# Kernel optimization log

Measured on AMD Instinct MI355X. Metric: run time of the kernel, lower is better.

Reference implementation:

```python
import jax, jax.numpy as jnp
import numpy as np
import math

B, S, D, H, F, E, K, L, V = 1, 2048, 768, 12, 1536, 8, 2, 2, 32000


def _ln(x, w, b, eps=1e-5):
    m = x.mean(-1, keepdims=True)
    v = ((x - m) ** 2).mean(-1, keepdims=True)
    return (x - m) / jnp.sqrt(v + eps) * w + b


def setup_inputs() -> dict:
    key = jax.random.key(0)
    ks = jax.random.split(key, 16)
    std = 0.02
    inp = {
        'tokens': jax.random.randint(ks[0], (B, S), 0, V),
        'emb': jax.random.normal(ks[1], (V, D), jnp.float32) * std,
        'qkv_w': jax.random.normal(ks[2], (L, 3 * D, D), jnp.float32) * std,
        'qkv_b': jax.random.normal(ks[3], (L, 3 * D), jnp.float32) * std,
        'out_w': jax.random.normal(ks[4], (L, D, D), jnp.float32) * std,
        'out_b': jax.random.normal(ks[5], (L, D), jnp.float32) * std,
        'ln1_w': jnp.ones((L, D), jnp.float32),
        'ln1_b': jax.random.normal(ks[6], (L, D), jnp.float32) * std,
        'ln2_w': jnp.ones((L, D), jnp.float32),
        'ln2_b': jax.random.normal(ks[7], (L, D), jnp.float32) * std,
        'gate_w': jax.random.normal(ks[8], (L, E, D), jnp.float32) * std,
        'eg_w': jax.random.normal(ks[9], (L, E, F, D), jnp.float32) * std,
        'eu_w': jax.random.normal(ks[10], (L, E, F, D), jnp.float32) * std,
        'ed_w': jax.random.normal(ks[11], (L, E, D, F), jnp.float32) * std,
        'rms_w': jnp.ones((D,), jnp.float32),
    }
    return inp


def reference(tokens, emb, qkv_w, qkv_b, out_w, out_b, ln1_w, ln1_b,
              ln2_w, ln2_b, gate_w, eg_w, eu_w, ed_w, rms_w):
    Dh = D // H
    x = emb[tokens] * math.sqrt(D)  # (B,S,D)
    for l in range(L):
        # --- MultiheadAttention (batch_first, no mask, eval) ---
        qkv = x @ qkv_w[l].T + qkv_b[l]
        q, k, v = jnp.split(qkv, 3, axis=-1)
        q = q.reshape(B, S, H, Dh).transpose(0, 2, 1, 3)
        k = k.reshape(B, S, H, Dh).transpose(0, 2, 1, 3)
        v = v.reshape(B, S, H, Dh).transpose(0, 2, 1, 3)
        att = jax.nn.softmax(jnp.einsum('bhqd,bhkd->bhqk', q, k) / math.sqrt(Dh), axis=-1)
        o = jnp.einsum('bhqk,bhkd->bhqd', att, v).transpose(0, 2, 1, 3).reshape(B, S, D)
        o = o @ out_w[l].T + out_b[l]
        x = _ln(x + o, ln1_w[l], ln1_b[l])
        # --- SimpleDeepseekV3MoE: top-k gate, softmax over top-k scores ---
        gs = jnp.einsum('bsd,ed->bse', x, gate_w[l])
        topv, topi = jax.lax.top_k(gs, K)
        tw = jax.nn.softmax(topv, axis=-1)  # (B,S,K)
        # dense per-expert combine weight (0 for unselected experts)
        ew = jnp.sum(jax.nn.one_hot(topi, E, dtype=x.dtype) * tw[..., None], axis=-2)  # (B,S,E)
        hg = jax.nn.silu(jnp.einsum('bsd,efd->bsef', x, eg_w[l]))
        hu = jnp.einsum('bsd,efd->bsef', x, eu_w[l])
        ye = jnp.einsum('bsef,edf->bsed', hg * hu, ed_w[l])
        moe = jnp.einsum('bsed,bse->bsd', ye, ew)
        x = _ln(x + moe, ln2_w[l], ln2_b[l])
    # final RMSNorm (torch default eps=None -> finfo eps)
    rms = jnp.sqrt(jnp.mean(x * x, axis=-1, keepdims=True) + jnp.finfo(x.dtype).eps)
    x = x / rms * rms_w
    logits = x @ emb.T  # tied lm_head
    return logits
```

## Files before the change

### kernel.cpp

```cpp
#include <hip/hip_runtime.h>

#define SQ   2048
#define DM   768
#define NHD  12
#define DHD  64
#define FF   1536
#define NE   8
#define NL   2
#define NV   32000

typedef __attribute__((ext_vector_type(8))) short bf16x8;
typedef __attribute__((ext_vector_type(4))) float f32x4;

__device__ __forceinline__ unsigned short f2bf(float f) {
  unsigned u = __float_as_uint(f);
  return (unsigned short)((u + 0x7fffu + ((u >> 16) & 1u)) >> 16);
}
__device__ __forceinline__ float bf2f(unsigned short h) {
  return __uint_as_float(((unsigned)h) << 16);
}

#define GLD16(ldsp, gp) __builtin_amdgcn_global_load_lds( \
    (const __attribute__((address_space(1))) void*)(gp),  \
    (__attribute__((address_space(3))) void*)(ldsp), 16, 0, 0)

__device__ __forceinline__ void conv8(const float* s, unsigned short* d) {
  float4 a = *(const float4*)s;
  float4 b = *(const float4*)(s + 4);
  int4 pk = make_int4(
      (int)((unsigned)f2bf(a.x) | ((unsigned)f2bf(a.y) << 16)),
      (int)((unsigned)f2bf(a.z) | ((unsigned)f2bf(a.w) << 16)),
      (int)((unsigned)f2bf(b.x) | ((unsigned)f2bf(b.y) << 16)),
      (int)((unsigned)f2bf(b.z) | ((unsigned)f2bf(b.w) << 16)));
  *(int4*)d = pk;
}

__global__ __launch_bounds__(256) void conv_k(const float* __restrict__ s,
    unsigned short* __restrict__ d) {
  size_t i = (size_t)(blockIdx.x * 256 + threadIdx.x) * 8;
  conv8(s + i, d + i);
}

__global__ __launch_bounds__(256) void conv3_k(const float* __restrict__ s0,
    const float* __restrict__ s1, const float* __restrict__ s2,
    unsigned short* __restrict__ d, int per) {
  int b = blockIdx.x;
  const float* s = (b < per) ? s0 : (b < 2 * per) ? s1 : s2;
  int sb = (b < per) ? b : (b < 2 * per) ? b - per : b - 2 * per;
  size_t di = (size_t)b * 2048 + threadIdx.x * 8;
  size_t si = (size_t)sb * 2048 + threadIdx.x * 8;
  conv8(s + si, d + di);
}

__global__ __launch_bounds__(256) void conv2_k(const float* __restrict__ s0,
    const float* __restrict__ s1, unsigned short* __restrict__ d, int per0) {
  int b = blockIdx.x;
  const float* s = (b < per0) ? s0 : s1;
  int sb = (b < per0) ? b : b - per0;
  size_t di = (size_t)b * 2048 + threadIdx.x * 8;
  size_t si = (size_t)sb * 2048 + threadIdx.x * 8;
  conv8(s + si, d + di);
}

__global__ __launch_bounds__(256) void embed_k(const int* __restrict__ tok,
    const float* __restrict__ emb, float* __restrict__ x,
    unsigned short* __restrict__ xbf, int* __restrict__ cnt) {
  if (blockIdx.x == 0 && threadIdx.x < NE) cnt[threadIdx.x] = 0;
  int idx = blockIdx.x * 256 + threadIdx.x;
  int s = idx / DM, d = idx % DM;
  float v = emb[(size_t)tok[s] * DM + d] * 27.712812921102035f;
  x[idx] = v;
  xbf[idx] = f2bf(v);
}

__global__ __launch_bounds__(512, 1) void gemmr_k(
    const unsigned short* __restrict__ A, long long lda,
    const unsigned short* __restrict__ B, long long ldb,
    float* __restrict__ C, long long ldc,
    int Kd, int mT)
{
  int nwg = gridDim.x, bid = blockIdx.x;
  int q = nwg >> 3, r = nwg & 7;
  int xcd = bid & 7, j = bid >> 3;
  int wid = (xcd < r ? xcd * (q + 1) : r * (q + 1) + (xcd - r) * q) + j;
  int mt = wid % mT, nt = wid / mT;
  int m0 = mt * 256, n0 = nt * 256;

  __shared__ __align__(16) unsigned short lds[4][2][8192];

  int t = threadIdx.x, w = t >> 6, lane = t & 63;
  int wm = w >> 2, wn = w & 3;
  int fr = lane & 15, ksg = lane >> 4;

  int srow = t >> 2;
  int schunk = ((t & 3) ^ ((srow >> 1) & 3)) * 8;
  const unsigned short* sa0 = A + (size_t)(m0 +       srow) * lda + schunk;
  const unsigned short* sa1 = A + (size_t)(m0 + 128 + srow) * lda + schunk;
  const unsigned short* sb0 = B + (size_t)(n0 +       srow) * ldb + schunk;
  const unsigned short* sb1 = B + (size_t)(n0 + 128 + srow) * ldb + schunk;
  int wofs = w * 512;

  int NS = Kd >> 5;
  f32x4 acc[8][4] = {};

#define STAGEV(s) { \
    int sl_ = (s) & 3; \
    long long ko_ = (long long)((s) >> 1) * 64 + ((s) & 1) * 32; \
    GLD16(&lds[sl_][0][wofs], sa0 + ko_); \
    GLD16(&lds[sl_][0][4096 + wofs], sa1 + ko_); \
    GLD16(&lds[sl_][1][wofs], sb0 + ko_); \
    GLD16(&lds[sl_][1][4096 + wofs], sb1 + ko_); }

  STAGEV(0);
  STAGEV(1);
  asm volatile("s_waitcnt vmcnt(4)" ::: "memory");
  __builtin_amdgcn_s_barrier();
  __builtin_amdgcn_sched_barrier(0);

  int ko = (ksg ^ ((fr >> 1) & 3)) * 8;
  for (int s = 0; s < NS; ++s) {
    int slot = s & 3;
    const unsigned short* Al = &lds[slot][0][0];
    const unsigned short* Bl = &lds[slot][1][0];
    bf16x8 af[8], bf[4];
    #pragma unroll
    for (int m = 0; m < 8; ++m)
      af[m] = *(const bf16x8*)&Al[(wm * 128 + m * 16 + fr) * 32 + ko];
    #pragma unroll
    for (int n = 0; n < 4; ++n)
      bf[n] = *(const bf16x8*)&Bl[(wn * 64 + n * 16 + fr) * 32 + ko];
    if (s + 2 < NS) STAGEV(s + 2);
    asm volatile("s_waitcnt lgkmcnt(0)" ::: "memory");
    __builtin_amdgcn_sched_barrier(0);
    __builtin_amdgcn_s_setprio(1);
    #pragma unroll
    for (int m = 0; m < 8; ++m)
      #pragma unroll
      for (int n = 0; n < 4; ++n)
        acc[m][n] = __builtin_amdgcn_mfma_f32_16x16x32_bf16(
            af[m], bf[n], acc[m][n], 0, 0, 0);
    __builtin_amdgcn_s_setprio(0);
    if (s + 1 < NS) {
      if (s + 2 < NS) asm volatile("s_waitcnt vmcnt(4)" ::: "memory");
      else            asm volatile("s_waitcnt vmcnt(0)" ::: "memory");
      __builtin_amdgcn_s_barrier();
      __builtin_amdgcn_sched_barrier(0);
    }
  }
#undef STAGEV

  int rb = ksg * 4;
  #pragma unroll
  for (int M = 0; M < 8; ++M)
    #pragma unroll
    for (int n = 0; n < 4; ++n)
      #pragma unroll
      for (int rr = 0; rr < 4; ++rr)
        C[(size_t)(m0 + wm * 128 + M * 16 + rb + rr) * ldc +
          (n0 + wn * 64 + n * 16 + fr)] = acc[M][n][rr];
}

template<bool GATHER, bool OBF16>
__global__ __launch_bounds__(512) void gemm256_k(
    const unsigned short* __restrict__ A, long long lda,
    const unsigned short* __restrict__ B, long long ldb, long long b_z,
    void* __restrict__ C, long long ldc, long long c_z,
    int M, int Kd, int mT, int nT, int Z, int zmod,
    const int* __restrict__ glist, long long gl_z,
    const int* __restrict__ cnt)
{
  int nwg = gridDim.x, bid = blockIdx.x;
  int q = nwg >> 3, r = nwg & 7;
  int xcd = bid & 7, j = bid >> 3;
  int wid = (xcd < r ? xcd * (q + 1) : r * (q + 1) + (xcd - r) * q) + j;
  int z = wid % Z; int rem = wid / Z;
  int mt = rem % mT, nt = rem / mT;
  int zz = z % zmod;
  int Mz = cnt ? cnt[zz] : M;
  int m0 = mt * 128, n0 = nt * 256;
  if (m0 >= Mz) return;
  (void)nT;

  const unsigned short* Bz = B + (size_t)z * b_z;

  __shared__ __align__(16) unsigned short lds[3 * 6 * 4096];

  int t = threadIdx.x, w = t >> 6, lane = t & 63;
  int wm = (w >> 2) * 64, wn = (w & 3) * 64;
  int fr = lane & 15, ksg = lane >> 4;
  int lrow = lane >> 3;
  int lchunk = ((lane & 7) ^ lrow) * 8;

  const unsigned short* sp[6];
  #pragma unroll
  for (int hh = 0; hh < 2; ++hh) {
    int gr = m0 + hh * 64 + w * 8 + lrow; if (gr >= Mz) gr = Mz - 1;
    int arow;
    if constexpr (GATHER) arow = glist[(size_t)zz * gl_z + gr]; else arow = gr;
    sp[hh] = A + (size_t)arow * lda + lchunk;
  }
  #pragma unroll
  for (int hh = 0; hh < 4; ++hh)
    sp[2 + hh] = Bz + (size_t)(n0 + hh * 64 + w * 8 + lrow) * ldb + lchunk;

  int rdA = (w >> 2) * 4096;
  int rdB = (2 + (w & 3)) * 4096;
  int stDst = w * 512;

  int rx = fr & 7;
  int off0 = (ksg ^ rx) * 8;
  int off1 = ((4 + ksg) ^ rx) * 8;

  int KT = Kd >> 6;
  f32x4 acc[4][4] = {};

  #pragma unroll
  for (int h = 0; h < 6; ++h)
    GLD16(&lds[h * 4096 + stDst], sp[h]);
  #pragma unroll
  for (int h = 0; h < 6; ++h)
    GLD16(&lds[(6 + h) * 4096 + stDst], sp[h] + 64);
  asm volatile("s_waitcnt vmcnt(6)" ::: "memory");
  __builtin_amdgcn_s_barrier();
  __builtin_amdgcn_sched_barrier(0);

  int buf = 0;
  for (int kt = 0; kt < KT; ++kt) {
    const unsigned short* Abl = &lds[buf * 6 * 4096 + rdA];
    const unsigned short* Bbl = &lds[buf * 6 * 4096 + rdB];
    int pf = (kt + 2 < KT);
    int pbuf = buf + 2; if (pbuf >= 3) pbuf -= 3;
    unsigned short* pd = &lds[pbuf * 6 * 4096 + stDst];
    long long koff = (long long)(kt + 2) * 64;

    if (pf) {
      GLD16(pd + 0 * 4096, sp[0] + koff);
      GLD16(pd + 1 * 4096, sp[1] + koff);
      GLD16(pd + 2 * 4096, sp[2] + koff);
    }
    {
      bf16x8 af[4], bv[4];
      #pragma unroll
      for (int m = 0; m < 4; ++m)
        af[m] = *(const bf16x8*)&Abl[(m * 16 + fr) * 64 + off0];
      #pragma unroll
      for (int n = 0; n < 4; ++n)
        bv[n] = *(const bf16x8*)&Bbl[(n * 16 + fr) * 64 + off0];
      __builtin_amdgcn_s_setprio(1);
      #pragma unroll
      for (int m = 0; m < 4; ++m)
        #pragma unroll
        for (int n = 0; n < 4; ++n)
          acc[m][n] = __builtin_amdgcn_mfma_f32_16x16x32_bf16(
              af[m], bv[n], acc[m][n], 0, 0, 0);
      __builtin_amdgcn_s_setprio(0);
    }
    if (pf) {
      GLD16(pd + 3 * 4096, sp[3] + koff);
      GLD16(pd + 4 * 4096, sp[4] + koff);
      GLD16(pd + 5 * 4096, sp[5] + koff);
    }
    {
      bf16x8 af[4], bv[4];
      #pragma unroll
      for (int m = 0; m < 4; ++m)
        af[m] = *(const bf16x8*)&Abl[(m * 16 + fr) * 64 + off1];
      #pragma unroll
      for (int n = 0; n < 4; ++n)
        bv[n] = *(const bf16x8*)&Bbl[(n * 16 + fr) * 64 + off1];
      __builtin_amdgcn_s_setprio(1);
      #pragma unroll
      for (int m = 0; m < 4; ++m)
        #pragma unroll
        for (int n = 0; n < 4; ++n)
          acc[m][n] = __builtin_amdgcn_mfma_f32_16x16x32_bf16(
              af[m], bv[n], acc[m][n], 0, 0, 0);
      __builtin_amdgcn_s_setprio(0);
    }
    if (pf) {
      asm volatile("s_waitcnt vmcnt(6)" ::: "memory");
    } else if (kt + 1 < KT) {
      asm volatile("s_waitcnt vmcnt(0)" ::: "memory");
    }
    __builtin_amdgcn_s_barrier();
    __builtin_amdgcn_sched_barrier(0);
    buf = buf + 1; if (buf == 3) buf = 0;
  }

  int rb = ksg * 4;
  #pragma unroll
  for (int m = 0; m < 4; ++m) {
    #pragma unroll
    for (int n = 0; n < 4; ++n) {
      #pragma unroll
      for (int rr = 0; rr < 4; ++rr) {
        int row = m0 + wm + m * 16 + rb + rr;
        if (row >= Mz) continue;
        size_t off = (size_t)z * c_z + (size_t)row * ldc +
                     (n0 + wn + n * 16 + fr);
        if constexpr (OBF16) ((unsigned short*)C)[off] = f2bf(acc[m][n][rr]);
        else                 ((float*)C)[off] = acc[m][n][rr];
      }
    }
  }
}

template<bool GATHER, bool BIAS, bool OBF16, bool VT>
__global__ __launch_bounds__(256) void gemm_k(
    const unsigned short* __restrict__ A, long long lda, long long a_z,
    const unsigned short* __restrict__ B, long long ldb, long long b_z,
    const float* __restrict__ bias,
    void* __restrict__ C, long long ldc, long long c_z,
    int M, int N, int Kd, float scale,
    const int* __restrict__ glist, long long gl_z,
    const int* __restrict__ cnt, int mT, int nT, int Z,
    unsigned short* __restrict__ vtout)
{
  int nwg = gridDim.x, bid = blockIdx.x;
  int q = nwg >> 3, r = nwg & 7;
  int xcd = bid & 7, j = bid >> 3;
  int wid = (xcd < r ? xcd * (q + 1) : r * (q + 1) + (xcd - r) * q) + j;
  int z = wid % Z; int rem = wid / Z;
  int mt = rem % mT, nt = rem / mT;

  int Mz = cnt ? cnt[z] : M;
  int m0 = mt * 128, n0 = nt * 128;
  if (m0 >= Mz) return;

  const unsigned short* Ab = A + (size_t)z * a_z;
  const unsigned short* Bb = B + (size_t)z * b_z;

  __shared__ __align__(16) unsigned short As[128 * 64];
  __shared__ __align__(16) unsigned short Bs[128 * 64];

  int t = threadIdx.x, w = t >> 6, lane = t & 63;
  int wm = (w >> 1) * 64, wn = (w & 1) * 64;
  int fr = lane & 15, ksg = lane >> 4;
  int lrow = lane >> 3;
  int lchunk = ((lane & 7) ^ lrow) * 8;

  const unsigned short* ap[4];
  const unsigned short* bp[4];
  unsigned short* la[4];
  unsigned short* lb[4];
  #pragma unroll
  for (int i = 0; i < 4; ++i) {
    int rrow = w * 32 + i * 8 + lrow;
    int gr = m0 + rrow; if (gr >= Mz) gr = Mz - 1;
    int arow; if constexpr (GATHER) arow = glist[(size_t)z * gl_z + gr]; else arow = gr;
    ap[i] = Ab + (size_t)arow * lda + lchunk;
    int br = n0 + rrow; if (br >= N) br = N - 1;
    bp[i] = Bb + (size_t)br * ldb + lchunk;
    la[i] = &As[(w * 32 + i * 8) * 64];
    lb[i] = &Bs[(w * 32 + i * 8) * 64];
  }

  int rx = fr & 7;
  int off0 = ((0 + ksg) ^ rx) * 8;
  int off1 = ((4 + ksg) ^ rx) * 8;

  f32x4 acc[4][4] = {};

  for (int k0 = 0; k0 < Kd; k0 += 64) {
    #pragma unroll
    for (int i = 0; i < 4; ++i) GLD16(la[i], ap[i] + k0);
    #pragma unroll
    for (int i = 0; i < 4; ++i) GLD16(lb[i], bp[i] + k0);
    __syncthreads();
    #pragma unroll
    for (int kb = 0; kb < 2; ++kb) {
      int offk = kb ? off1 : off0;
      bf16x8 af[4], bv[4];
      #pragma unroll
      for (int m = 0; m < 4; ++m)
        af[m] = *(const bf16x8*)&As[(wm + m * 16 + fr) * 64 + offk];
      #pragma unroll
      for (int n = 0; n < 4; ++n)
        bv[n] = *(const bf16x8*)&Bs[(wn + n * 16 + fr) * 64 + offk];
      #pragma unroll
      for (int m = 0; m < 4; ++m)
        #pragma unroll
        for (int n = 0; n < 4; ++n)
          acc[m][n] = __builtin_amdgcn_mfma_f32_16x16x32_bf16(
              af[m], bv[n], acc[m][n], 0, 0, 0);
    }
    __syncthreads();
  }

  int rb = ksg * 4;
  #pragma unroll
  for (int m = 0; m < 4; ++m) {
    #pragma unroll
    for (int n = 0; n < 4; ++n) {
      int col = n0 + wn + n * 16 + fr;
      if (col >= N) continue;
      #pragma unroll
      for (int rr = 0; rr < 4; ++rr) {
        int row = m0 + wm + m * 16 + rb + rr;
        if (row >= Mz) continue;
        float v = acc[m][n][rr] * scale;
        if constexpr (BIAS) v += bias[col];
        size_t off = (size_t)z * c_z + (size_t)row * ldc + col;
        if constexpr (OBF16) ((unsigned short*)C)[off] = f2bf(v);
        else                 ((float*)C)[off] = v;
        if constexpr (VT) {
          if (n0 >= 2 * DM)
            vtout[(size_t)(col - 2 * DM) * SQ + row] = f2bf(v);
        }
      }
    }
  }
}

__global__ __launch_bounds__(128) void flash_k(
    const unsigned short* __restrict__ qkv,
    const unsigned short* __restrict__ vt,
    unsigned short* __restrict__ o)
{
  int nwg = gridDim.x, bid = blockIdx.x;
  int cpx = nwg >> 3;
  int wid = (bid & 7) * cpx + (bid >> 3);
  int h  = wid >> 6;
  int qt = wid & 63;
  int q0 = qt * 32;

  __shared__ __align__(16) unsigned short Ks[128 * 64];
  __shared__ __align__(16) unsigned short Vs[128 * 64];
  __shared__ __align__(16) unsigned short Ps[2][16 * 136];

  int t = threadIdx.x, w = t >> 6, lane = t & 63;
  int fr = lane & 15, ksg = lane >> 4;
  int lrow = lane >> 3;
  int lchunk = ((lane & 7) ^ lrow) * 8;

  const unsigned short* qbase = qkv + (size_t)q0 * (3 * DM) + h * DHD;
  #pragma unroll
  for (int i = 0; i < 2; ++i) {
    int rrow = w * 16 + i * 8 + lrow;
    GLD16(&Ks[(w * 16 + i * 8) * 64], qbase + (size_t)rrow * (3 * DM) + lchunk);
  }
  __syncthreads();
  bf16x8 qf[2];
  {
    int row = w * 16 + fr, ph = fr & 7;
    qf[0] = *(const bf16x8*)&Ks[row * 64 + ((ksg ^ ph) * 8)];
    qf[1] = *(const bf16x8*)&Ks[row * 64 + (((4 + ksg) ^ ph) * 8)];
  }
  __syncthreads();

  const unsigned short* kbase = qkv + DM + h * DHD;
  const unsigned short* vb = vt + (size_t)(h * DHD) * SQ;

  f32x4 oacc[4] = {};
  float m_r[4] = {-1e30f, -1e30f, -1e30f, -1e30f};
  float l_r[4] = {0.f, 0.f, 0.f, 0.f};

  for (int kt = 0; kt < SQ / 128; ++kt) {
    int kk0 = kt * 128;
    #pragma unroll
    for (int i = 0; i < 8; ++i) {
      int rrow = w * 64 + i * 8 + lrow;
      GLD16(&Ks[(w * 64 + i * 8) * 64],
            kbase + (size_t)(kk0 + rrow) * (3 * DM) + lchunk);
    }
    #pragma unroll
    for (int i = 0; i < 8; ++i) {
      int p = w * 64 + i * 8 + lrow;
      GLD16(&Vs[(w * 64 + i * 8) * 64],
            vb + (size_t)(p >> 1) * SQ + kk0 + (p & 1) * 64 + lchunk);
    }
    __syncthreads();

    f32x4 sacc[8] = {};
    #pragma unroll
    for (int kb = 0; kb < 2; ++kb) {
      #pragma unroll
      for (int n = 0; n < 8; ++n) {
        int row = n * 16 + fr;
        bf16x8 bvv = *(const bf16x8*)&Ks[row * 64 +
            (((kb * 4 + ksg) ^ (fr & 7)) * 8)];
        sacc[n] = __builtin_amdgcn_mfma_f32_16x16x32_bf16(
            qf[kb], bvv, sacc[n], 0, 0, 0);
      }
    }

    #pragma unroll
    for (int r = 0; r < 4; ++r) {
      float mx = sacc[0][r];
      #pragma unroll
      for (int n = 1; n < 8; ++n) mx = fmaxf(mx, sacc[n][r]);
      mx = fmaxf(mx, __shfl_xor(mx, 1));
      mx = fmaxf(mx, __shfl_xor(mx, 2));
      mx = fmaxf(mx, __shfl_xor(mx, 4));
      mx = fmaxf(mx, __shfl_xor(mx, 8));
      float mn = fmaxf(m_r[r], mx * 0.125f);
      float resc = __expf(m_r[r] - mn);
      m_r[r] = mn;
      #pragma unroll
      for (int n = 0; n < 4; ++n) oacc[n][r] *= resc;
      float rs = 0.f;
      #pragma unroll
      for (int n = 0; n < 8; ++n) {
        float p = __expf(sacc[n][r] * 0.125f - mn);
        rs += p;
        Ps[w][(ksg * 4 + r) * 136 + n * 16 + fr] = f2bf(p);
      }
      rs += __shfl_xor(rs, 1);
      rs += __shfl_xor(rs, 2);
      rs += __shfl_xor(rs, 4);
      rs += __shfl_xor(rs, 8);
      l_r[r] = l_r[r] * resc + rs;
    }

    #pragma unroll
    for (int ksi = 0; ksi < 4; ++ksi) {
      bf16x8 pa = *(const bf16x8*)&Ps[w][fr * 136 + ksi * 32 + ksg * 8];
      #pragma unroll
      for (int n = 0; n < 4; ++n) {
        int p = (n * 16 + fr) * 2 + (ksi >> 1);
        int c = (ksi & 1) * 4 + ksg;
        bf16x8 bvv = *(const bf16x8*)&Vs[p * 64 + ((c ^ (p & 7)) * 8)];
        oacc[n] = __builtin_amdgcn_mfma_f32_16x16x32_bf16(
            pa, bvv, oacc[n], 0, 0, 0);
      }
    }
    __syncthreads();
  }

  unsigned short* ob = o + (size_t)(q0 + w * 16) * DM + h * DHD;
  #pragma unroll
  for (int r = 0; r < 4; ++r) {
    float invl = 1.f / l_r[r];
    int qrow = ksg * 4 + r;
    #pragma unroll
    for (int n = 0; n < 4; ++n)
      ob[(size_t)qrow * DM + n * 16 + fr] = f2bf(oacc[n][r] * invl);
  }
}

__global__ __launch_bounds__(256) void add_ln_gate_k(const float* __restrict__ xin,
    const float* __restrict__ add, const float* __restrict__ w,
    const float* __restrict__ b, const float* __restrict__ gw,
    float* __restrict__ xout, unsigned short* __restrict__ xbf,
    float* __restrict__ tw, int* __restrict__ ti, int* __restrict__ cnt,
    int* __restrict__ lists, int* __restrict__ slot) {
  int row = blockIdx.x, t = threadIdx.x;
  const float* xi = xin + (size_t)row * DM;
  const float* ai = add + (size_t)row * DM;
  float v[3]; float s = 0.f, sq = 0.f;
  #pragma unroll
  for (int i = 0; i < 3; ++i) {
    int idx = t + i * 256;
    v[i] = xi[idx] + ai[idx];
    s += v[i]; sq += v[i] * v[i];
  }
  #pragma unroll
  for (int o = 32; o; o >>= 1) { s += __shfl_xor(s, o); sq += __shfl_xor(sq, o); }
  __shared__ float rsm[4], rqm[4];
  __shared__ float gsm[4][NE];
  int wv = t >> 6, lane = t & 63;
  if (lane == 0) { rsm[wv] = s; rqm[wv] = sq; }
  __syncthreads();
  s = rsm[0] + rsm[1] + rsm[2] + rsm[3];
  sq = rqm[0] + rqm[1] + rqm[2] + rqm[3];
  float mean = s * (1.f / 768.f);
  float var = sq * (1.f / 768.f) - mean * mean;
  float inv = rsqrtf(var + 1e-5f);
  float* xo = xout + (size_t)row * DM;
  unsigned short* xb = xbf + (size_t)row * DM;
  float y[3];
  #pragma unroll
  for (int i = 0; i < 3; ++i) {
    int idx = t + i * 256;
    y[i] = (v[i] - mean) * inv * w[idx] + b[idx];
    xo[idx] = y[i]; xb[idx] = f2bf(y[i]);
  }
  float p[NE];
  #pragma unroll
  for (int e = 0; e < NE; ++e) {
    p[e] = y[0] * gw[e * DM + t] + y[1] * gw[e * DM + t + 256]
         + y[2] * gw[e * DM + t + 512];
    #pragma unroll
    for (int o = 32; o; o >>= 1) p[e] += __shfl_xor(p[e], o);
  }
  if (lane == 0) {
    #pragma unroll
    for (int e = 0; e < NE; ++e) gsm[wv][e] = p[e];
  }
  __syncthreads();
  if (t == 0) {
    float v0 = -1e30f, v1 = -1e30f; int i0 = 0, i1 = 0;
    #pragma unroll
    for (int e = 0; e < NE; ++e) {
      float g = gsm[0][e] + gsm[1][e] + gsm[2][e] + gsm[3][e];
      if (g > v0) { v1 = v0; i1 = i0; v0 = g; i0 = e; }
      else if (g > v1) { v1 = g; i1 = e; }
    }
    float e1 = expf(v1 - v0);
    float invs = 1.f / (1.f + e1);
    tw[row * 2] = invs; tw[row * 2 + 1] = e1 * invs;
    ti[row * 2] = i0;   ti[row * 2 + 1] = i1;
    int p0 = atomicAdd(&cnt[i0], 1); lists[i0 * SQ + p0] = row; slot[row * 2] = p0;
    int p1 = atomicAdd(&cnt[i1], 1); lists[i1 * SQ + p1] = row; slot[row * 2 + 1] = p1;
  }
}

__global__ __launch_bounds__(256) void silu_mul_k(unsigned short* __restrict__ hg,
    const unsigned short* __restrict__ hu, const int* __restrict__ cnt) {
  int e = blockIdx.y, sl = blockIdx.x;
  if (sl >= cnt[e]) return;
  size_t base = ((size_t)e * SQ + sl) * FF;
  int t = threadIdx.x;
  #pragma unroll
  for (int i = 0; i < FF / 256; ++i) {
    size_t idx = base + t + i * 256;
    float g = bf2f(hg[idx]);
    float u = bf2f(hu[idx]);
    float sv = g / (1.f + expf(-g));
    hg[idx] = f2bf(sv * u);
  }
}

__global__ __launch_bounds__(256) void combine_ln_k(const float* __restrict__ xin,
    const float* __restrict__ ye, const float* __restrict__ tw,
    const int* __restrict__ ti, const int* __restrict__ slot,
    const float* __restrict__ w, const float* __restrict__ b,
    float* __restrict__ xout, unsigned short* __restrict__ xbf,
    int* __restrict__ cnt) {
  int row = blockIdx.x, t = threadIdx.x;
  if (row < NE && t == 0) cnt[row] = 0;
  int e0 = ti[row * 2], e1 = ti[row * 2 + 1];
  int p0 = slot[row * 2], p1 = slot[row * 2 + 1];
  float w0 = tw[row * 2], w1 = tw[row * 2 + 1];
  const float* y0 = ye + ((size_t)e0 * SQ + p0) * DM;
  const float* y1 = ye + ((size_t)e1 * SQ + p1) * DM;
  const float* xi = xin + (size_t)row * DM;
  float v[3]; float s = 0.f, sq = 0.f;
  #pragma unroll
  for (int i = 0; i < 3; ++i) {
    int idx = t + i * 256;
    v[i] = xi[idx] + w0 * y0[idx] + w1 * y1[idx];
    s += v[i]; sq += v[i] * v[i];
  }
  #pragma unroll
  for (int o = 32; o; o >>= 1) { s += __shfl_xor(s, o); sq += __shfl_xor(sq, o); }
  __shared__ float rsm[4], rqm[4];
  int wv = t >> 6;
  if ((t & 63) == 0) { rsm[wv] = s; rqm[wv] = sq; }
  __syncthreads();
  s = rsm[0] + rsm[1] + rsm[2] + rsm[3];
  sq = rqm[0] + rqm[1] + rqm[2] + rqm[3];
  float mean = s * (1.f / 768.f);
  float var = sq * (1.f / 768.f) - mean * mean;
  float inv = rsqrtf(var + 1e-5f);
  float* xo = xout + (size_t)row * DM;
  unsigned short* xb = xbf + (size_t)row * DM;
  #pragma unroll
  for (int i = 0; i < 3; ++i) {
    int idx = t + i * 256;
    float y = (v[i] - mean) * inv * w[idx] + b[idx];
    xo[idx] = y; xb[idx] = f2bf(y);
  }
}

__global__ __launch_bounds__(256) void rms_k(const float* __restrict__ x,
    const float* __restrict__ rw, unsigned short* __restrict__ xbf) {
  int row = blockIdx.x, t = threadIdx.x;
  const float* xi = x + (size_t)row * DM;
  float v[3]; float sq = 0.f;
  #pragma unroll
  for (int i = 0; i < 3; ++i) {
    int idx = t + i * 256;
    v[i] = xi[idx];
    sq += v[i] * v[i];
  }
  #pragma unroll
  for (int o = 32; o; o >>= 1) sq += __shfl_xor(sq, o);
  __shared__ float rqm[4];
  int wv = t >> 6;
  if ((t & 63) == 0) rqm[wv] = sq;
  __syncthreads();
  sq = rqm[0] + rqm[1] + rqm[2] + rqm[3];
  float inv = rsqrtf(sq * (1.f / 768.f) + 1.1920929e-07f);
  unsigned short* xb = xbf + (size_t)row * DM;
  #pragma unroll
  for (int i = 0; i < 3; ++i) {
    int idx = t + i * 256;
    xb[idx] = f2bf(v[i] * inv * rw[idx]);
  }
}

extern "C" void kernel_launch(void* const* d_in, const int* in_sizes, int n_in,
                              void* d_out, int out_size, void* d_ws, size_t ws_size,
                              hipStream_t stream) {
  (void)in_sizes; (void)n_in; (void)out_size; (void)ws_size;
  const int*   tokens = (const int*)d_in[0];
  const float* emb    = (const float*)d_in[1];
  const float* qkv_w  = (const float*)d_in[2];
  const float* qkv_b  = (const float*)d_in[3];
  const float* out_w  = (const float*)d_in[4];
  const float* out_b  = (const float*)d_in[5];
  const float* ln1_w  = (const float*)d_in[6];
  const float* ln1_b  = (const float*)d_in[7];
  const float* ln2_w  = (const float*)d_in[8];
  const float* ln2_b  = (const float*)d_in[9];
  const float* gate_w = (const float*)d_in[10];
  const float* eg_w   = (const float*)d_in[11];
  const float* eu_w   = (const float*)d_in[12];
  const float* ed_w   = (const float*)d_in[13];
  const float* rms_w  = (const float*)d_in[14];
  float* out = (float*)d_out;

  char* wsb = (char*)d_ws;
  float*          x_f    = (float*)(wsb + 0);
  unsigned short* x_bf   = (unsigned short*)(wsb + 6291456);
  unsigned short* qkv_bf = (unsigned short*)(wsb + 9437184);
  unsigned short* vt     = (unsigned short*)(wsb + 18874368);
  unsigned short* o_bf   = (unsigned short*)(wsb + 22020096);
  float*          tmp_f  = (float*)(wsb + 25165824);
  float*          tw     = (float*)(wsb + 31457280);
  int*            ti     = (int*)(wsb + 31473664);
  int*            cnt    = (int*)(wsb + 31490048);
  int*            lists  = (int*)(wsb + 31490304);
  int*            slot   = (int*)(wsb + 31555840);
  unsigned short* emb_bf = (unsigned short*)(wsb + 31572224);
  unsigned short* wbf    = (unsigned short*)(wsb + 80724224);
  unsigned short* hg     = (unsigned short*)(wsb + 142065920);
  unsigned short* hu     = (unsigned short*)(wsb + 142065920 + 50331648);
  float*          ye     = (float*)(wsb + 142065920 + 50331648);

  unsigned short* qw_bf = wbf;
  unsigned short* ow_bf = wbf + 1769472;
  unsigned short* eg_bf = wbf + 2359296;
  unsigned short* ed_bf = wbf + 21233664;

  conv_k<<<12000, 256, 0, stream>>>(emb, emb_bf);
  embed_k<<<SQ * DM / 256, 256, 0, stream>>>(tokens, emb, x_f, x_bf, cnt);

  for (int l = 0; l < NL; ++l) {
    const float* qw = qkv_w + (size_t)l * 3 * DM * DM;
    const float* qb = qkv_b + (size_t)l * 3 * DM;
    const float* ob = out_b + (size_t)l * DM;
    const float* ow = out_w + (size_t)l * DM * DM;
    const float* gw = gate_w + (size_t)l * NE * DM;
    const float* egw = eg_w + (size_t)l * NE * FF * DM;
    const float* euw = eu_w + (size_t)l * NE * FF * DM;
    const float* edw = ed_w + (size_t)l * NE * DM * FF;

    conv2_k<<<1152, 256, 0, stream>>>(qw, ow, qw_bf, 864);
    conv3_k<<<13824, 256, 0, stream>>>(egw, euw, edw, eg_bf, 4608);

    gemm_k<false, true, true, true><<<16 * 18, 256, 0, stream>>>(
        x_bf, DM, 0, qw_bf, DM, 0, qb, qkv_bf, 3 * DM, 0,
        SQ, 3 * DM, DM, 1.f, nullptr, 0, nullptr, 16, 18, 1, vt);

    flash_k<<<NHD * 64, 128, 0, stream>>>(qkv_bf, vt, o_bf);

    gemm_k<false, true, false, false><<<16 * 6, 256, 0, stream>>>(
        o_bf, DM, 0, ow_bf, DM, 0, ob, tmp_f, DM, 0,
        SQ, DM, DM, 1.f, nullptr, 0, nullptr, 16, 6, 1, nullptr);

    add_ln_gate_k<<<SQ, 256, 0, stream>>>(x_f, tmp_f, ln1_w + l * DM,
        ln1_b + l * DM, gw, x_f, x_bf, tw, ti, cnt, lists, slot);

    gemm256_k<true, true><<<16 * 6 * 16, 512, 0, stream>>>(
        x_bf, DM, eg_bf, DM, (long long)FF * DM,
        hg, FF, (long long)SQ * FF,
        SQ, DM, 16, 6, 16, 8, lists, SQ, cnt);

    silu_mul_k<<<dim3(SQ, NE), 256, 0, stream>>>(hg, hu, cnt);

    gemm_k<false, false, false, false><<<16 * 6 * NE, 256, 0, stream>>>(
        hg, FF, (long long)SQ * FF, ed_bf, FF, (long long)DM * FF, nullptr,
        ye, DM, (long long)SQ * DM,
        SQ, DM, FF, 1.f, nullptr, 0, cnt, 16, 6, NE, nullptr);

    combine_ln_k<<<SQ, 256, 0, stream>>>(x_f, ye, tw, ti, slot,
                                         ln2_w + l * DM, ln2_b + l * DM,
                                         x_f, x_bf, cnt);
  }

  rms_k<<<SQ, 256, 0, stream>>>(x_f, rms_w, x_bf);

  gemmr_k<<<8 * 125, 512, 0, stream>>>(
      x_bf, DM, emb_bf, DM, out, NV, DM, 8);
}
```

Before: 783.0 us.

## Batch weight conversion, move QKV and down-proj to 256-wide GEMM, fuse RMSNorm

Weight fp32->bf16 conversion for both layers is hoisted into single upfront launches instead of per-layer launches. The QKV projection and expert down-projection now use the larger 256-column tile GEMM, which gains bias and V-transpose epilogue support. silu_mul is collapsed to one block per row that loops over experts. The final RMSNorm is fused into the last combine+LayerNorm kernel. The intent is fewer launches and better GEMM efficiency. The trade-offs are larger workspace use and fewer workgroups for the down-projection grid.

```diff
diff --git a/kernel.cpp b/kernel.cpp
--- a/kernel.cpp
+++ b/kernel.cpp
@@ -41,12 +41,15 @@
   conv8(s + i, d + i);
 }
 
-__global__ __launch_bounds__(256) void conv3_k(const float* __restrict__ s0,
+__global__ __launch_bounds__(256) void conv4_k(const float* __restrict__ s0,
     const float* __restrict__ s1, const float* __restrict__ s2,
-    unsigned short* __restrict__ d, int per) {
+    const float* __restrict__ s3, unsigned short* __restrict__ d, int per) {
   int b = blockIdx.x;
-  const float* s = (b < per) ? s0 : (b < 2 * per) ? s1 : s2;
-  int sb = (b < per) ? b : (b < 2 * per) ? b - per : b - 2 * per;
+  const float* s; int sb;
+  if (b < per)          { s = s0; sb = b; }
+  else if (b < 2 * per) { s = s1; sb = b - per; }
+  else if (b < 3 * per) { s = s2; sb = b - 2 * per; }
+  else                  { s = s3; sb = b - 3 * per; }
   size_t di = (size_t)b * 2048 + threadIdx.x * 8;
   size_t si = (size_t)sb * 2048 + threadIdx.x * 8;
   conv8(s + si, d + di);
@@ -160,11 +163,13 @@
           (n0 + wn * 64 + n * 16 + fr)] = acc[M][n][rr];
 }
 
-template<bool GATHER, bool OBF16>
+template<bool GATHER, bool OBF16, bool BIAS, bool VT>
 __global__ __launch_bounds__(512) void gemm256_k(
-    const unsigned short* __restrict__ A, long long lda,
+    const unsigned short* __restrict__ A, long long lda, long long a_z,
     const unsigned short* __restrict__ B, long long ldb, long long b_z,
+    const float* __restrict__ bias,
     void* __restrict__ C, long long ldc, long long c_z,
+    unsigned short* __restrict__ vtout,
     int M, int Kd, int mT, int nT, int Z, int zmod,
     const int* __restrict__ glist, long long gl_z,
     const int* __restrict__ cnt)
@@ -181,6 +186,7 @@
   if (m0 >= Mz) return;
   (void)nT;
 
+  const unsigned short* Az = A + (size_t)z * a_z;
   const unsigned short* Bz = B + (size_t)z * b_z;
 
   __shared__ __align__(16) unsigned short lds[3 * 6 * 4096];
@@ -197,7 +203,7 @@
     int gr = m0 + hh * 64 + w * 8 + lrow; if (gr >= Mz) gr = Mz - 1;
     int arow;
     if constexpr (GATHER) arow = glist[(size_t)zz * gl_z + gr]; else arow = gr;
-    sp[hh] = A + (size_t)arow * lda + lchunk;
+    sp[hh] = Az + (size_t)arow * lda + lchunk;
   }
   #pragma unroll
   for (int hh = 0; hh < 4; ++hh)
@@ -292,20 +298,26 @@
   for (int m = 0; m < 4; ++m) {
     #pragma unroll
     for (int n = 0; n < 4; ++n) {
+      int col = n0 + wn + n * 16 + fr;
       #pragma unroll
       for (int rr = 0; rr < 4; ++rr) {
         int row = m0 + wm + m * 16 + rb + rr;
         if (row >= Mz) continue;
-        size_t off = (size_t)z * c_z + (size_t)row * ldc +
-                     (n0 + wn + n * 16 + fr);
-        if constexpr (OBF16) ((unsigned short*)C)[off] = f2bf(acc[m][n][rr]);
-        else                 ((float*)C)[off] = acc[m][n][rr];
+        float v = acc[m][n][rr];
+        if constexpr (BIAS) v += bias[col];
+        size_t off = (size_t)z * c_z + (size_t)row * ldc + col;
+        if constexpr (OBF16) ((unsigned short*)C)[off] = f2bf(v);
+        else                 ((float*)C)[off] = v;
+        if constexpr (VT) {
+          if (n0 >= 2 * DM)
+            vtout[(size_t)(col - 2 * DM) * SQ + row] = f2bf(v);
+        }
       }
     }
   }
 }
 
-template<bool GATHER, bool BIAS, bool OBF16, bool VT>
+template<bool GATHER, bool BIAS, bool OBF16>
 __global__ __launch_bounds__(256) void gemm_k(
     const unsigned short* __restrict__ A, long long lda, long long a_z,
     const unsigned short* __restrict__ B, long long ldb, long long b_z,
@@ -313,8 +325,7 @@
     void* __restrict__ C, long long ldc, long long c_z,
     int M, int N, int Kd, float scale,
     const int* __restrict__ glist, long long gl_z,
-    const int* __restrict__ cnt, int mT, int nT, int Z,
-    unsigned short* __restrict__ vtout)
+    const int* __restrict__ cnt, int mT, int nT, int Z)
 {
   int nwg = gridDim.x, bid = blockIdx.x;
   int q = nwg >> 3, r = nwg & 7;
@@ -403,10 +414,6 @@
         size_t off = (size_t)z * c_z + (size_t)row * ldc + col;
         if constexpr (OBF16) ((unsigned short*)C)[off] = f2bf(v);
         else                 ((float*)C)[off] = v;
-        if constexpr (VT) {
-          if (n0 >= 2 * DM)
-            vtout[(size_t)(col - 2 * DM) * SQ + row] = f2bf(v);
-        }
       }
     }
   }
@@ -607,28 +614,32 @@
 
 __global__ __launch_bounds__(256) void silu_mul_k(unsigned short* __restrict__ hg,
     const unsigned short* __restrict__ hu, const int* __restrict__ cnt) {
-  int e = blockIdx.y, sl = blockIdx.x;
-  if (sl >= cnt[e]) return;
-  size_t base = ((size_t)e * SQ + sl) * FF;
-  int t = threadIdx.x;
-  #pragma unroll
-  for (int i = 0; i < FF / 256; ++i) {
-    size_t idx = base + t + i * 256;
-    float g = bf2f(hg[idx]);
-    float u = bf2f(hu[idx]);
-    float sv = g / (1.f + expf(-g));
-    hg[idx] = f2bf(sv * u);
-  }
-}
-
+  int sl = blockIdx.x, t = threadIdx.x;
+  for (int e = 0; e < NE; ++e) {
+    if (sl < cnt[e]) {
+      size_t base = ((size_t)e * SQ + sl) * FF;
+      #pragma unroll
+      for (int i = 0; i < FF / 256; ++i) {
+        size_t idx = base + t + i * 256;
+        float g = bf2f(hg[idx]);
+        float u = bf2f(hu[idx]);
+        float sv = g / (1.f + expf(-g));
+        hg[idx] = f2bf(sv * u);
+      }
+    }
+  }
+}
+
+template<bool FINAL>
 __global__ __launch_bounds__(256) void combine_ln_k(const float* __restrict__ xin,
     const float* __restrict__ ye, const float* __restrict__ tw,
     const int* __restrict__ ti, const int* __restrict__ slot,
     const float* __restrict__ w, const float* __restrict__ b,
+    const float* __restrict__ rw,
     float* __restrict__ xout, unsigned short* __restrict__ xbf,
     int* __restrict__ cnt) {
   int row = blockIdx.x, t = threadIdx.x;
-  if (row < NE && t == 0) cnt[row] = 0;
+  if (!FINAL && row < NE && t == 0) cnt[row] = 0;
   int e0 = ti[row * 2], e1 = ti[row * 2 + 1];
   int p0 = slot[row * 2], p1 = slot[row * 2 + 1];
   float w0 = tw[row * 2], w1 = tw[row * 2 + 1];
@@ -653,40 +664,34 @@
   float mean = s * (1.f / 768.f);
   float var = sq * (1.f / 768.f) - mean * mean;
   float inv = rsqrtf(var + 1e-5f);
-  float* xo = xout + (size_t)row * DM;
   unsigned short* xb = xbf + (size_t)row * DM;
+  float y[3];
   #pragma unroll
   for (int i = 0; i < 3; ++i) {
     int idx = t + i * 256;
-    float y = (v[i] - mean) * inv * w[idx] + b[idx];
-    xo[idx] = y; xb[idx] = f2bf(y);
-  }
-}
-
-__global__ __launch_bounds__(256) void rms_k(const float* __restrict__ x,
-    const float* __restrict__ rw, unsigned short* __restrict__ xbf) {
-  int row = blockIdx.x, t = threadIdx.x;
-  const float* xi = x + (size_t)row * DM;
-  float v[3]; float sq = 0.f;
-  #pragma unroll
-  for (int i = 0; i < 3; ++i) {
-    int idx = t + i * 256;
-    v[i] = xi[idx];
-    sq += v[i] * v[i];
-  }
-  #pragma unroll
-  for (int o = 32; o; o >>= 1) sq += __shfl_xor(sq, o);
-  __shared__ float rqm[4];
-  int wv = t >> 6;
-  if ((t & 63) == 0) rqm[wv] = sq;
-  __syncthreads();
-  sq = rqm[0] + rqm[1] + rqm[2] + rqm[3];
-  float inv = rsqrtf(sq * (1.f / 768.f) + 1.1920929e-07f);
-  unsigned short* xb = xbf + (size_t)row * DM;
-  #pragma unroll
-  for (int i = 0; i < 3; ++i) {
-    int idx = t + i * 256;
-    xb[idx] = f2bf(v[i] * inv * rw[idx]);
+    y[i] = (v[i] - mean) * inv * w[idx] + b[idx];
+  }
+  if constexpr (!FINAL) {
+    float* xo = xout + (size_t)row * DM;
+    #pragma unroll
+    for (int i = 0; i < 3; ++i) {
+      int idx = t + i * 256;
+      xo[idx] = y[i]; xb[idx] = f2bf(y[i]);
+    }
+  } else {
+    float sq2 = y[0] * y[0] + y[1] * y[1] + y[2] * y[2];
+    #pragma unroll
+    for (int o = 32; o; o >>= 1) sq2 += __shfl_xor(sq2, o);
+    __syncthreads();
+    if ((t & 63) == 0) rqm[wv] = sq2;
+    __syncthreads();
+    sq2 = rqm[0] + rqm[1] + rqm[2] + rqm[3];
+    float inv2 = rsqrtf(sq2 * (1.f / 768.f) + 1.1920929e-07f);
+    #pragma unroll
+    for (int i = 0; i < 3; ++i) {
+      int idx = t + i * 256;
+      xb[idx] = f2bf(y[i] * inv2 * rw[idx]);
+    }
   }
 }
 
@@ -725,62 +730,64 @@
   int*            slot   = (int*)(wsb + 31555840);
   unsigned short* emb_bf = (unsigned short*)(wsb + 31572224);
   unsigned short* wbf    = (unsigned short*)(wsb + 80724224);
-  unsigned short* hg     = (unsigned short*)(wsb + 142065920);
-  unsigned short* hu     = (unsigned short*)(wsb + 142065920 + 50331648);
-  float*          ye     = (float*)(wsb + 142065920 + 50331648);
-
-  unsigned short* qw_bf = wbf;
-  unsigned short* ow_bf = wbf + 1769472;
-  unsigned short* eg_bf = wbf + 2359296;
-  unsigned short* ed_bf = wbf + 21233664;
-
+  unsigned short* hg     = (unsigned short*)(wsb + 203407616);
+  unsigned short* hu     = (unsigned short*)(wsb + 203407616 + 50331648);
+  float*          ye     = (float*)(wsb + 203407616 + 50331648);
+
+  unsigned short* qw_all  = wbf;
+  unsigned short* ow_all  = wbf + 3538944;
+  unsigned short* egu_all = wbf + 4718592;
+  unsigned short* ed_all  = wbf + 42467328;
+
+  conv2_k<<<2304, 256, 0, stream>>>(qkv_w, out_w, qw_all, 1728);
+  conv4_k<<<18432, 256, 0, stream>>>(eg_w, eu_w,
+      eg_w + (size_t)NE * FF * DM, eu_w + (size_t)NE * FF * DM,
+      egu_all, 4608);
+  conv_k<<<9216, 256, 0, stream>>>(ed_w, ed_all);
   conv_k<<<12000, 256, 0, stream>>>(emb, emb_bf);
   embed_k<<<SQ * DM / 256, 256, 0, stream>>>(tokens, emb, x_f, x_bf, cnt);
 
   for (int l = 0; l < NL; ++l) {
-    const float* qw = qkv_w + (size_t)l * 3 * DM * DM;
     const float* qb = qkv_b + (size_t)l * 3 * DM;
     const float* ob = out_b + (size_t)l * DM;
-    const float* ow = out_w + (size_t)l * DM * DM;
     const float* gw = gate_w + (size_t)l * NE * DM;
-    const float* egw = eg_w + (size_t)l * NE * FF * DM;
-    const float* euw = eu_w + (size_t)l * NE * FF * DM;
-    const float* edw = ed_w + (size_t)l * NE * DM * FF;
-
-    conv2_k<<<1152, 256, 0, stream>>>(qw, ow, qw_bf, 864);
-    conv3_k<<<13824, 256, 0, stream>>>(egw, euw, edw, eg_bf, 4608);
-
-    gemm_k<false, true, true, true><<<16 * 18, 256, 0, stream>>>(
-        x_bf, DM, 0, qw_bf, DM, 0, qb, qkv_bf, 3 * DM, 0,
-        SQ, 3 * DM, DM, 1.f, nullptr, 0, nullptr, 16, 18, 1, vt);
+    unsigned short* qw_l  = qw_all + (size_t)l * 1769472;
+    unsigned short* ow_l  = ow_all + (size_t)l * 589824;
+    unsigned short* egu_l = egu_all + (size_t)l * 18874368;
+    unsigned short* ed_l  = ed_all + (size_t)l * 9437184;
+
+    gemm256_k<false, true, true, true><<<16 * 9, 512, 0, stream>>>(
+        x_bf, DM, 0, qw_l, DM, 0, qb, qkv_bf, 3 * DM, 0, vt,
+        SQ, DM, 16, 9, 1, 1, nullptr, 0, nullptr);
 
     flash_k<<<NHD * 64, 128, 0, stream>>>(qkv_bf, vt, o_bf);
 
-    gemm_k<false, true, false, false><<<16 * 6, 256, 0, stream>>>(
-        o_bf, DM, 0, ow_bf, DM, 0, ob, tmp_f, DM, 0,
-        SQ, DM, DM, 1.f, nullptr, 0, nullptr, 16, 6, 1, nullptr);
+    gemm_k<false, true, false><<<16 * 6, 256, 0, stream>>>(
+        o_bf, DM, 0, ow_l, DM, 0, ob, tmp_f, DM, 0,
+        SQ, DM, DM, 1.f, nullptr, 0, nullptr, 16, 6, 1);
 
     add_ln_gate_k<<<SQ, 256, 0, stream>>>(x_f, tmp_f, ln1_w + l * DM,
         ln1_b + l * DM, gw, x_f, x_bf, tw, ti, cnt, lists, slot);
 
-    gemm256_k<true, true><<<16 * 6 * 16, 512, 0, stream>>>(
-        x_bf, DM, eg_bf, DM, (long long)FF * DM,
-        hg, FF, (long long)SQ * FF,
+    gemm256_k<true, true, false, false><<<16 * 6 * 16, 512, 0, stream>>>(
+        x_bf, DM, 0, egu_l, DM, (long long)FF * DM, nullptr,
+        hg, FF, (long long)SQ * FF, nullptr,
         SQ, DM, 16, 6, 16, 8, lists, SQ, cnt);
 
-    silu_mul_k<<<dim3(SQ, NE), 256, 0, stream>>>(hg, hu, cnt);
-
-    gemm_k<false, false, false, false><<<16 * 6 * NE, 256, 0, stream>>>(
-        hg, FF, (long long)SQ * FF, ed_bf, FF, (long long)DM * FF, nullptr,
-        ye, DM, (long long)SQ * DM,
-        SQ, DM, FF, 1.f, nullptr, 0, cnt, 16, 6, NE, nullptr);
-
-    combine_ln_k<<<SQ, 256, 0, stream>>>(x_f, ye, tw, ti, slot,
-                                         ln2_w + l * DM, ln2_b + l * DM,
-                                         x_f, x_bf, cnt);
-  }
-
-  rms_k<<<SQ, 256, 0, stream>>>(x_f, rms_w, x_bf);
+    silu_mul_k<<<SQ, 256, 0, stream>>>(hg, hu, cnt);
+
+    gemm256_k<false, false, false, false><<<16 * 3 * 8, 512, 0, stream>>>(
+        hg, FF, (long long)SQ * FF, ed_l, FF, (long long)DM * FF, nullptr,
+        ye, DM, (long long)SQ * DM, nullptr,
+        SQ, FF, 16, 3, 8, 8, nullptr, 0, cnt);
+
+    if (l == NL - 1)
+      combine_ln_k<true><<<SQ, 256, 0, stream>>>(x_f, ye, tw, ti, slot,
+          ln2_w + l * DM, ln2_b + l * DM, rms_w, x_f, x_bf, cnt);
+    else
+      combine_ln_k<false><<<SQ, 256, 0, stream>>>(x_f, ye, tw, ti, slot,
+          ln2_w + l * DM, ln2_b + l * DM, rms_w, x_f, x_bf, cnt);
+  }
 
   gemmr_k<<<8 * 125, 512, 0, stream>>>(
       x_bf, DM, emb_bf, DM, out, NV, DM, 8);
```

New measurement: 815.6 us. 4.2% more time.
